# Kernel optimization log

Measured on AMD Instinct MI355X. Metric: run time of the kernel, lower is better.

The kernel has to match this reference:

```python
import jax, jax.numpy as jnp
import numpy as np

HEADS = 16  # config.heads


def setup_inputs() -> dict:
    key = jax.random.key(0)
    k1, k2, k3, k4 = jax.random.split(key, 4)
    B, S, H = 2, 2048, 2048
    x = jax.random.normal(k1, (B, S, H), dtype=jnp.float32)
    w_qkv = jax.random.normal(k2, (H, 3 * H), dtype=jnp.float32) * 0.02
    b_qkv = jax.random.normal(k3, (3 * H,), dtype=jnp.float32) * 0.02
    w_o = jax.random.normal(k4, (H, H), dtype=jnp.float32) * 0.02
    return {"x": x, "w_qkv": w_qkv, "b_qkv": b_qkv, "w_o": w_o}


def reference(x, w_qkv, b_qkv, w_o):
    # pre_layer_norm=False path: plain linear QKV projection
    B, S, H = x.shape
    hd = H // HEADS  # head_size
    scale = 1.0 / jnp.sqrt(jnp.float32(hd))  # 1/norm_factor^2, use_mup=False
    qkv = x @ w_qkv + b_qkv  # [B, S, 3H]
    q, k, v = qkv[..., :H], qkv[..., H:2 * H], qkv[..., 2 * H:]

    def split_heads(t):  # [B,S,H] -> [B,heads,S,hd]
        return t.reshape(B, S, HEADS, hd).transpose(0, 2, 1, 3)

    qh, kh, vh = split_heads(q), split_heads(k), split_heads(v)
    # score_4d_matmul with triangular masking + scale
    scores = jnp.einsum('bhqd,bhkd->bhqk', qh, kh) * scale  # [B,h,S,S]
    causal = jnp.tril(jnp.ones((S, S), dtype=bool))
    scores = jnp.where(causal, scores, -jnp.inf)
    probs = jax.nn.softmax(scores, axis=-1)
    # context_4d_matmul -> merge heads back to [B,S,H]
    ctx = jnp.einsum('bhqk,bhkd->bhqd', probs, vh)
    ctx = ctx.transpose(0, 2, 1, 3).reshape(B, S, H)
    # vector_matmul with attn_ow (no bias in this path)
    out = ctx @ w_o
    return out
```

## Files before the change

### kernel.cpp

```cpp
#include <hip/hip_runtime.h>
#include <cstdint>
#include <cstddef>

typedef __attribute__((ext_vector_type(8))) short bf16x8;
typedef __attribute__((ext_vector_type(4))) float f32x4;
typedef __attribute__((ext_vector_type(4))) unsigned short ushort4_;

#define MFMA16(a, b, c) __builtin_amdgcn_mfma_f32_16x16x32_bf16((a), (b), (c), 0, 0, 0)

__device__ __forceinline__ unsigned short f2bf(float f) {
  union { float f; unsigned u; } c; c.f = f;
  unsigned r = c.u + 0x7fffu + ((c.u >> 16) & 1u);
  return (unsigned short)(r >> 16);
}

__device__ __forceinline__ void gl_lds16(const unsigned short* g, unsigned short* l) {
  __builtin_amdgcn_global_load_lds(
      (const __attribute__((address_space(1))) void*)g,
      (__attribute__((address_space(3))) void*)l, 16, 0, 0);
}

__global__ __launch_bounds__(256) void k_cvt(const float* __restrict__ x,
                                             unsigned short* __restrict__ y) {
  int i = blockIdx.x * 256 + threadIdx.x;
  float4 v = reinterpret_cast<const float4*>(x)[i];
  ushort4_ o;
  o.x = f2bf(v.x); o.y = f2bf(v.y); o.z = f2bf(v.z); o.w = f2bf(v.w);
  reinterpret_cast<ushort4_*>(y)[i] = o;
}

__global__ __launch_bounds__(256) void k_transpose_cvt(const float* __restrict__ W,
                                                       unsigned short* __restrict__ WT,
                                                       int N) {
  __shared__ unsigned short t[64][65];
  const int n0 = blockIdx.x * 64;
  const int k0 = blockIdx.y * 64;
  const int tid = threadIdx.x;
#pragma unroll
  for (int i = 0; i < 16; i++) {
    int li = tid + i * 256;
    int kk = li >> 6, nn = li & 63;
    t[kk][nn] = f2bf(W[(size_t)(k0 + kk) * N + (n0 + nn)]);
  }
  __syncthreads();
#pragma unroll
  for (int i = 0; i < 16; i++) {
    int li = tid + i * 256;
    int nn = li >> 6, kk = li & 63;
    WT[(size_t)(n0 + nn) * 2048 + (k0 + kk)] = t[kk][nn];
  }
}

template <int MODE>
__global__ __launch_bounds__(256) void k_gemm(const unsigned short* __restrict__ A,
                                              const unsigned short* __restrict__ Bt,
                                              const float* __restrict__ bias,
                                              unsigned short* __restrict__ qb,
                                              unsigned short* __restrict__ kb,
                                              unsigned short* __restrict__ vtb,
                                              float* __restrict__ outp) {
  __shared__ __align__(16) unsigned short As[128 * 64];
  __shared__ __align__(16) unsigned short Bs[128 * 64];
  const int tid = threadIdx.x;
  const int lane = tid & 63, wid = tid >> 6;
  const int quad = lane >> 4, l16 = lane & 15;
  const int wm = wid >> 1, wn = wid & 1;
  const int m0 = blockIdx.y * 128, n0 = blockIdx.x * 128;

  f32x4 acc[4][4];
#pragma unroll
  for (int i = 0; i < 4; i++)
#pragma unroll
    for (int j = 0; j < 4; j++) {
      f32x4 z = {0.f, 0.f, 0.f, 0.f};
      acc[i][j] = z;
    }

  for (int k0 = 0; k0 < 2048; k0 += 64) {
    __syncthreads();
#pragma unroll
    for (int i = 0; i < 4; i++) {
      int slotbase = wid * 64 + i * 256;
      int slot = slotbase + lane;
      int row = slot >> 3, chs = slot & 7, gch = chs ^ (row & 7);
      gl_lds16(A + (size_t)(m0 + row) * 2048 + k0 + gch * 8, &As[slotbase * 8]);
      gl_lds16(Bt + (size_t)(n0 + row) * 2048 + k0 + gch * 8, &Bs[slotbase * 8]);
    }
    __syncthreads();
#pragma unroll
    for (int kc = 0; kc < 2; kc++) {
      bf16x8 af[4], bfr[4];
#pragma unroll
      for (int mt = 0; mt < 4; mt++) {
        int r = wm * 64 + mt * 16 + l16;
        int ch = kc * 4 + quad;
        af[mt] = *reinterpret_cast<const bf16x8*>(&As[r * 64 + ((ch ^ (r & 7)) * 8)]);
      }
#pragma unroll
      for (int nt = 0; nt < 4; nt++) {
        int r = wn * 64 + nt * 16 + l16;
        int ch = kc * 4 + quad;
        bfr[nt] = *reinterpret_cast<const bf16x8*>(&Bs[r * 64 + ((ch ^ (r & 7)) * 8)]);
      }
#pragma unroll
      for (int mt = 0; mt < 4; mt++)
#pragma unroll
        for (int nt = 0; nt < 4; nt++)
          acc[mt][nt] = MFMA16(af[mt], bfr[nt], acc[mt][nt]);
    }
  }

  const int mbase = m0 + wm * 64;
  const int nbase = n0 + wn * 64;
  if (MODE == 0) {
#pragma unroll
    for (int nt = 0; nt < 4; nt++) {
      int n = nbase + nt * 16 + l16;
      float bv = bias[n];
      int seg = n >> 11;
      int h = (n >> 7) & 15;
      int d = n & 127;
#pragma unroll
      for (int mt = 0; mt < 4; mt++) {
        int mrow = mbase + mt * 16 + quad * 4;
        int b = mrow >> 11, s = mrow & 2047;
        if (seg == 2) {
          ushort4_ pk;
          pk.x = f2bf(acc[mt][nt][0] + bv);
          pk.y = f2bf(acc[mt][nt][1] + bv);
          pk.z = f2bf(acc[mt][nt][2] + bv);
          pk.w = f2bf(acc[mt][nt][3] + bv);
          *reinterpret_cast<ushort4_*>(vtb + ((size_t)(b * 16 + h) * 128 + d) * 2048 + s) = pk;
        } else {
          unsigned short* dst = (seg == 0 ? qb : kb);
          size_t base = (size_t)(b * 16 + h) * 2048;
#pragma unroll
          for (int rg = 0; rg < 4; rg++)
            dst[(base + (s + rg)) * 128 + d] = f2bf(acc[mt][nt][rg] + bv);
        }
      }
    }
  } else {
#pragma unroll
    for (int nt = 0; nt < 4; nt++) {
      int n = nbase + nt * 16 + l16;
#pragma unroll
      for (int mt = 0; mt < 4; mt++) {
        int mrow = mbase + mt * 16 + quad * 4;
#pragma unroll
        for (int rg = 0; rg < 4; rg++)
          outp[(size_t)(mrow + rg) * 2048 + n] = acc[mt][nt][rg];
      }
    }
  }
}

__global__ __launch_bounds__(512) void k_attn(const unsigned short* __restrict__ qb,
                                              const unsigned short* __restrict__ kb,
                                              const unsigned short* __restrict__ vtb,
                                              unsigned short* __restrict__ ctx) {
  __shared__ __align__(16) unsigned short Ks[2][64 * 128];
  __shared__ __align__(16) unsigned short Vs[2][128 * 64];
  __shared__ __align__(16) unsigned short Ps[128 * 64];
  const int qt = (gridDim.x - 1) - blockIdx.x;
  const int bh = blockIdx.y;
  const int tid = threadIdx.x;
  const int lane = tid & 63, w = tid >> 6;
  const int quad = lane >> 4, l16 = lane & 15;
  const int qbase = qt * 128;
  const unsigned short* Qh = qb + (size_t)bh * 2048 * 128;
  const unsigned short* Kh = kb + (size_t)bh * 2048 * 128;
  const unsigned short* Vh = vtb + (size_t)bh * 128 * 2048;

  const int q_lo = qbase + w * 16;
  const int nkv = 2 * qt + 2;
  const float sl2 = 0.12751741f;

  bf16x8 qf[4];
#pragma unroll
  for (int kc = 0; kc < 4; kc++)
    qf[kc] = *reinterpret_cast<const bf16x8*>(
        Qh + (size_t)(q_lo + l16) * 128 + kc * 32 + quad * 8);

  f32x4 o[8];
#pragma unroll
  for (int dt = 0; dt < 8; dt++) {
    f32x4 z = {0.f, 0.f, 0.f, 0.f};
    o[dt] = z;
  }
  float m_run = -1e30f, l_run = 0.f;

  auto stage = [&](int kvb, int bsel) {
    unsigned short* Kd = &Ks[bsel][0];
    unsigned short* Vd = &Vs[bsel][0];
#pragma unroll
    for (int i = 0; i < 2; i++) {
      int slotbase = i * 512 + w * 64;
      int slot = slotbase + lane;
      int rowk = slot >> 4, chk = (slot & 15) ^ (rowk & 7);
      gl_lds16(Kh + (size_t)(kvb + rowk) * 128 + chk * 8, Kd + slotbase * 8);
      int rowv = slot >> 3, chv = (slot & 7) ^ (rowv & 7);
      gl_lds16(Vh + (size_t)rowv * 2048 + kvb + chv * 8, Vd + slotbase * 8);
    }
  };

  stage(0, 0);

  for (int kv = 0; kv < nkv; kv++) {
    const int kvb = kv * 64;
    const int cur = kv & 1;
    asm volatile("s_waitcnt vmcnt(0)" ::: "memory");
    asm volatile("s_barrier" ::: "memory");
    if (kv + 1 < nkv) stage(kvb + 64, cur ^ 1);
    if (kvb > q_lo + 15) continue;

    const unsigned short* Kc = &Ks[cur][0];
    const unsigned short* Vc = &Vs[cur][0];

    f32x4 sacc[4];
#pragma unroll
    for (int nt = 0; nt < 4; nt++) {
      f32x4 z = {0.f, 0.f, 0.f, 0.f};
      sacc[nt] = z;
    }
#pragma unroll
    for (int kc = 0; kc < 4; kc++) {
      bf16x8 kf[4];
#pragma unroll
      for (int nt = 0; nt < 4; nt++) {
        int r = nt * 16 + l16, ch = kc * 4 + quad;
        kf[nt] = *reinterpret_cast<const bf16x8*>(&Kc[r * 128 + ((ch ^ (r & 7)) * 8)]);
      }
#pragma unroll
      for (int nt = 0; nt < 4; nt++)
        sacc[nt] = MFMA16(kf[nt], qf[kc], sacc[nt]);
    }

    const bool needmask = (kvb + 63) > q_lo;
    const int qabs = q_lo + l16;
    float tmax = -1e30f;
#pragma unroll
    for (int nt = 0; nt < 4; nt++)
#pragma unroll
      for (int rg = 0; rg < 4; rg++) {
        float v = sacc[nt][rg] * sl2;
        if (needmask && (kvb + nt * 16 + quad * 4 + rg) > qabs) v = -1e30f;
        sacc[nt][rg] = v;
        tmax = fmaxf(tmax, v);
      }
    tmax = fmaxf(tmax, __shfl_xor(tmax, 16));
    tmax = fmaxf(tmax, __shfl_xor(tmax, 32));
    float mnew = fmaxf(m_run, tmax);
    float alpha = exp2f(m_run - mnew);
    m_run = mnew;
    float rsum = 0.f;
#pragma unroll
    for (int nt = 0; nt < 4; nt++)
#pragma unroll
      for (int rg = 0; rg < 4; rg++) {
        float p = exp2f(sacc[nt][rg] - mnew);
        sacc[nt][rg] = p;
        rsum += p;
      }
    rsum += __shfl_xor(rsum, 16);
    rsum += __shfl_xor(rsum, 32);
    l_run = l_run * alpha + rsum;
#pragma unroll
    for (int dt = 0; dt < 8; dt++)
#pragma unroll
      for (int rg = 0; rg < 4; rg++) o[dt][rg] *= alpha;

#pragma unroll
    for (int nt = 0; nt < 4; nt++) {
      ushort4_ pk;
      pk.x = f2bf(sacc[nt][0]);
      pk.y = f2bf(sacc[nt][1]);
      pk.z = f2bf(sacc[nt][2]);
      pk.w = f2bf(sacc[nt][3]);
      int chunk = nt * 2 + (quad >> 1);
      *reinterpret_cast<ushort4_*>(
          &Ps[(w * 16 + l16) * 64 + ((chunk ^ (l16 & 7)) * 8) + (quad & 1) * 4]) = pk;
    }
    asm volatile("s_waitcnt lgkmcnt(0)" ::: "memory");

#pragma unroll
    for (int kc = 0; kc < 2; kc++) {
      int chunkr = kc * 4 + quad;
      bf16x8 pf = *reinterpret_cast<const bf16x8*>(
          &Ps[(w * 16 + l16) * 64 + ((chunkr ^ (l16 & 7)) * 8)]);
#pragma unroll
      for (int dt = 0; dt < 8; dt++) {
        int r = dt * 16 + l16, ch = kc * 4 + quad;
        bf16x8 vf = *reinterpret_cast<const bf16x8*>(&Vc[r * 64 + ((ch ^ (r & 7)) * 8)]);
        o[dt] = MFMA16(vf, pf, o[dt]);
      }
    }
  }

  const int b = bh >> 4, h = bh & 15;
  const float inv = 1.f / l_run;
  const int s = q_lo + l16;
#pragma unroll
  for (int dt = 0; dt < 8; dt++) {
    int d0 = dt * 16 + quad * 4;
    ushort4_ pk;
    pk.x = f2bf(o[dt][0] * inv);
    pk.y = f2bf(o[dt][1] * inv);
    pk.z = f2bf(o[dt][2] * inv);
    pk.w = f2bf(o[dt][3] * inv);
    *reinterpret_cast<ushort4_*>(
        &ctx[((size_t)b * 2048 + s) * 2048 + h * 128 + d0]) = pk;
  }
}

extern "C" void kernel_launch(void* const* d_in, const int* in_sizes, int n_in,
                              void* d_out, int out_size, void* d_ws, size_t ws_size,
                              hipStream_t stream) {
  const float* x = (const float*)d_in[0];
  const float* w_qkv = (const float*)d_in[1];
  const float* b_qkv = (const float*)d_in[2];
  const float* w_o = (const float*)d_in[3];
  float* outp = (float*)d_out;

  unsigned short* ws = (unsigned short*)d_ws;
  unsigned short* xb    = ws;
  unsigned short* wqkvT = xb + 8388608;
  unsigned short* woT   = wqkvT + 12582912;
  unsigned short* qbuf  = woT + 4194304;
  unsigned short* kbuf  = qbuf + 8388608;
  unsigned short* vtbuf = kbuf + 8388608;
  unsigned short* ctxb  = vtbuf + 8388608;

  k_cvt<<<8192, 256, 0, stream>>>(x, xb);
  k_transpose_cvt<<<dim3(96, 32), 256, 0, stream>>>(w_qkv, wqkvT, 6144);
  k_transpose_cvt<<<dim3(32, 32), 256, 0, stream>>>(w_o, woT, 2048);
  k_gemm<0><<<dim3(48, 32), 256, 0, stream>>>(xb, wqkvT, b_qkv, qbuf, kbuf, vtbuf, nullptr);
  k_attn<<<dim3(16, 32), 512, 0, stream>>>(qbuf, kbuf, vtbuf, ctxb);
  k_gemm<1><<<dim3(16, 32), 256, 0, stream>>>(ctxb, woT, nullptr, nullptr, nullptr, nullptr, outp);
}
```

Measured before the change: 425.1 us.

## Give each attention wave two query tiles; merge prep kernels into one launch

The attention kernel now runs 4 waves of 256 threads instead of 8. Each wave handles 32 query rows as two 16-row halves, so every K and V fragment read from LDS feeds two MFMAs, halving LDS traffic per FLOP. Staging loops are widened to match. The three conversion and transpose kernels are fused into a single k_prep launch to cut launch overhead. The cost is higher register pressure per wave and fewer waves per block to hide latency, with launch_bounds(256,2) asking for two blocks per CU.

```diff
diff --git a/kernel.cpp b/kernel.cpp
--- a/kernel.cpp
+++ b/kernel.cpp
@@ -20,22 +20,35 @@
       (__attribute__((address_space(3))) void*)l, 16, 0, 0);
 }
 
-__global__ __launch_bounds__(256) void k_cvt(const float* __restrict__ x,
-                                             unsigned short* __restrict__ y) {
-  int i = blockIdx.x * 256 + threadIdx.x;
-  float4 v = reinterpret_cast<const float4*>(x)[i];
-  ushort4_ o;
-  o.x = f2bf(v.x); o.y = f2bf(v.y); o.z = f2bf(v.z); o.w = f2bf(v.w);
-  reinterpret_cast<ushort4_*>(y)[i] = o;
-}
-
-__global__ __launch_bounds__(256) void k_transpose_cvt(const float* __restrict__ W,
-                                                       unsigned short* __restrict__ WT,
-                                                       int N) {
+__global__ __launch_bounds__(256) void k_prep(const float* __restrict__ x,
+                                              unsigned short* __restrict__ xb,
+                                              const float* __restrict__ wqkv,
+                                              unsigned short* __restrict__ wqkvT,
+                                              const float* __restrict__ wo,
+                                              unsigned short* __restrict__ woT) {
   __shared__ unsigned short t[64][65];
-  const int n0 = blockIdx.x * 64;
-  const int k0 = blockIdx.y * 64;
+  const int blk = blockIdx.x;
   const int tid = threadIdx.x;
+  if (blk < 8192) {
+    int i = blk * 256 + tid;
+    float4 v = reinterpret_cast<const float4*>(x)[i];
+    ushort4_ o;
+    o.x = f2bf(v.x); o.y = f2bf(v.y); o.z = f2bf(v.z); o.w = f2bf(v.w);
+    reinterpret_cast<ushort4_*>(xb)[i] = o;
+    return;
+  }
+  const float* W;
+  unsigned short* WT;
+  int n0, k0, N;
+  if (blk < 11264) {
+    int local = blk - 8192;
+    W = wqkv; WT = wqkvT; N = 6144;
+    n0 = (local % 96) * 64; k0 = (local / 96) * 64;
+  } else {
+    int local = blk - 11264;
+    W = wo; WT = woT; N = 2048;
+    n0 = (local % 32) * 64; k0 = (local / 32) * 64;
+  }
 #pragma unroll
   for (int i = 0; i < 16; i++) {
     int li = tid + i * 256;
@@ -155,10 +168,10 @@
   }
 }
 
-__global__ __launch_bounds__(512) void k_attn(const unsigned short* __restrict__ qb,
-                                              const unsigned short* __restrict__ kb,
-                                              const unsigned short* __restrict__ vtb,
-                                              unsigned short* __restrict__ ctx) {
+__global__ __launch_bounds__(256, 2) void k_attn(const unsigned short* __restrict__ qb,
+                                                 const unsigned short* __restrict__ kb,
+                                                 const unsigned short* __restrict__ vtb,
+                                                 unsigned short* __restrict__ ctx) {
   __shared__ __align__(16) unsigned short Ks[2][64 * 128];
   __shared__ __align__(16) unsigned short Vs[2][128 * 64];
   __shared__ __align__(16) unsigned short Ps[128 * 64];
@@ -172,30 +185,34 @@
   const unsigned short* Kh = kb + (size_t)bh * 2048 * 128;
   const unsigned short* Vh = vtb + (size_t)bh * 128 * 2048;
 
-  const int q_lo = qbase + w * 16;
+  const int q_lo = qbase + w * 32;
   const int nkv = 2 * qt + 2;
   const float sl2 = 0.12751741f;
 
-  bf16x8 qf[4];
-#pragma unroll
-  for (int kc = 0; kc < 4; kc++)
-    qf[kc] = *reinterpret_cast<const bf16x8*>(
-        Qh + (size_t)(q_lo + l16) * 128 + kc * 32 + quad * 8);
-
-  f32x4 o[8];
-#pragma unroll
-  for (int dt = 0; dt < 8; dt++) {
-    f32x4 z = {0.f, 0.f, 0.f, 0.f};
-    o[dt] = z;
-  }
-  float m_run = -1e30f, l_run = 0.f;
+  bf16x8 qf[2][4];
+#pragma unroll
+  for (int half = 0; half < 2; half++)
+#pragma unroll
+    for (int kc = 0; kc < 4; kc++)
+      qf[half][kc] = *reinterpret_cast<const bf16x8*>(
+          Qh + (size_t)(q_lo + half * 16 + l16) * 128 + kc * 32 + quad * 8);
+
+  f32x4 o[2][8];
+#pragma unroll
+  for (int half = 0; half < 2; half++)
+#pragma unroll
+    for (int dt = 0; dt < 8; dt++) {
+      f32x4 z = {0.f, 0.f, 0.f, 0.f};
+      o[half][dt] = z;
+    }
+  float m_run[2] = {-1e30f, -1e30f}, l_run[2] = {0.f, 0.f};
 
   auto stage = [&](int kvb, int bsel) {
     unsigned short* Kd = &Ks[bsel][0];
     unsigned short* Vd = &Vs[bsel][0];
 #pragma unroll
-    for (int i = 0; i < 2; i++) {
-      int slotbase = i * 512 + w * 64;
+    for (int i = 0; i < 4; i++) {
+      int slotbase = i * 256 + w * 64;
       int slot = slotbase + lane;
       int rowk = slot >> 4, chk = (slot & 15) ^ (rowk & 7);
       gl_lds16(Kh + (size_t)(kvb + rowk) * 128 + chk * 8, Kd + slotbase * 8);
@@ -212,104 +229,114 @@
     asm volatile("s_waitcnt vmcnt(0)" ::: "memory");
     asm volatile("s_barrier" ::: "memory");
     if (kv + 1 < nkv) stage(kvb + 64, cur ^ 1);
-    if (kvb > q_lo + 15) continue;
+    if (kvb > q_lo + 31) continue;
 
     const unsigned short* Kc = &Ks[cur][0];
     const unsigned short* Vc = &Vs[cur][0];
 
-    f32x4 sacc[4];
-#pragma unroll
-    for (int nt = 0; nt < 4; nt++) {
-      f32x4 z = {0.f, 0.f, 0.f, 0.f};
-      sacc[nt] = z;
-    }
+    f32x4 sacc[2][4];
+#pragma unroll
+    for (int half = 0; half < 2; half++)
+#pragma unroll
+      for (int nt = 0; nt < 4; nt++) {
+        f32x4 z = {0.f, 0.f, 0.f, 0.f};
+        sacc[half][nt] = z;
+      }
 #pragma unroll
     for (int kc = 0; kc < 4; kc++) {
-      bf16x8 kf[4];
 #pragma unroll
       for (int nt = 0; nt < 4; nt++) {
         int r = nt * 16 + l16, ch = kc * 4 + quad;
-        kf[nt] = *reinterpret_cast<const bf16x8*>(&Kc[r * 128 + ((ch ^ (r & 7)) * 8)]);
-      }
+        bf16x8 kf = *reinterpret_cast<const bf16x8*>(&Kc[r * 128 + ((ch ^ (r & 7)) * 8)]);
+        sacc[0][nt] = MFMA16(kf, qf[0][kc], sacc[0][nt]);
+        sacc[1][nt] = MFMA16(kf, qf[1][kc], sacc[1][nt]);
+      }
+    }
+
+    const bool needmask = (kvb + 63) > q_lo;
+#pragma unroll
+    for (int half = 0; half < 2; half++) {
+      const int qabs = q_lo + half * 16 + l16;
+      float tmax = -1e30f;
 #pragma unroll
       for (int nt = 0; nt < 4; nt++)
-        sacc[nt] = MFMA16(kf[nt], qf[kc], sacc[nt]);
-    }
-
-    const bool needmask = (kvb + 63) > q_lo;
-    const int qabs = q_lo + l16;
-    float tmax = -1e30f;
-#pragma unroll
-    for (int nt = 0; nt < 4; nt++)
-#pragma unroll
-      for (int rg = 0; rg < 4; rg++) {
-        float v = sacc[nt][rg] * sl2;
-        if (needmask && (kvb + nt * 16 + quad * 4 + rg) > qabs) v = -1e30f;
-        sacc[nt][rg] = v;
-        tmax = fmaxf(tmax, v);
-      }
-    tmax = fmaxf(tmax, __shfl_xor(tmax, 16));
-    tmax = fmaxf(tmax, __shfl_xor(tmax, 32));
-    float mnew = fmaxf(m_run, tmax);
-    float alpha = exp2f(m_run - mnew);
-    m_run = mnew;
-    float rsum = 0.f;
-#pragma unroll
-    for (int nt = 0; nt < 4; nt++)
-#pragma unroll
-      for (int rg = 0; rg < 4; rg++) {
-        float p = exp2f(sacc[nt][rg] - mnew);
-        sacc[nt][rg] = p;
-        rsum += p;
-      }
-    rsum += __shfl_xor(rsum, 16);
-    rsum += __shfl_xor(rsum, 32);
-    l_run = l_run * alpha + rsum;
-#pragma unroll
-    for (int dt = 0; dt < 8; dt++)
-#pragma unroll
-      for (int rg = 0; rg < 4; rg++) o[dt][rg] *= alpha;
-
-#pragma unroll
-    for (int nt = 0; nt < 4; nt++) {
-      ushort4_ pk;
-      pk.x = f2bf(sacc[nt][0]);
-      pk.y = f2bf(sacc[nt][1]);
-      pk.z = f2bf(sacc[nt][2]);
-      pk.w = f2bf(sacc[nt][3]);
-      int chunk = nt * 2 + (quad >> 1);
-      *reinterpret_cast<ushort4_*>(
-          &Ps[(w * 16 + l16) * 64 + ((chunk ^ (l16 & 7)) * 8) + (quad & 1) * 4]) = pk;
+#pragma unroll
+        for (int rg = 0; rg < 4; rg++) {
+          float v = sacc[half][nt][rg] * sl2;
+          if (needmask && (kvb + nt * 16 + quad * 4 + rg) > qabs) v = -1e30f;
+          sacc[half][nt][rg] = v;
+          tmax = fmaxf(tmax, v);
+        }
+      tmax = fmaxf(tmax, __shfl_xor(tmax, 16));
+      tmax = fmaxf(tmax, __shfl_xor(tmax, 32));
+      float mnew = fmaxf(m_run[half], tmax);
+      float alpha = exp2f(m_run[half] - mnew);
+      m_run[half] = mnew;
+      float rsum = 0.f;
+#pragma unroll
+      for (int nt = 0; nt < 4; nt++)
+#pragma unroll
+        for (int rg = 0; rg < 4; rg++) {
+          float p = exp2f(sacc[half][nt][rg] - mnew);
+          sacc[half][nt][rg] = p;
+          rsum += p;
+        }
+      rsum += __shfl_xor(rsum, 16);
+      rsum += __shfl_xor(rsum, 32);
+      l_run[half] = l_run[half] * alpha + rsum;
+#pragma unroll
+      for (int dt = 0; dt < 8; dt++)
+#pragma unroll
+        for (int rg = 0; rg < 4; rg++) o[half][dt][rg] *= alpha;
+
+#pragma unroll
+      for (int nt = 0; nt < 4; nt++) {
+        ushort4_ pk;
+        pk.x = f2bf(sacc[half][nt][0]);
+        pk.y = f2bf(sacc[half][nt][1]);
+        pk.z = f2bf(sacc[half][nt][2]);
+        pk.w = f2bf(sacc[half][nt][3]);
+        int chunk = nt * 2 + (quad >> 1);
+        *reinterpret_cast<ushort4_*>(
+            &Ps[(w * 32 + half * 16 + l16) * 64 + ((chunk ^ (l16 & 7)) * 8) +
+                (quad & 1) * 4]) = pk;
+      }
     }
     asm volatile("s_waitcnt lgkmcnt(0)" ::: "memory");
 
 #pragma unroll
     for (int kc = 0; kc < 2; kc++) {
       int chunkr = kc * 4 + quad;
-      bf16x8 pf = *reinterpret_cast<const bf16x8*>(
-          &Ps[(w * 16 + l16) * 64 + ((chunkr ^ (l16 & 7)) * 8)]);
+      bf16x8 pf0 = *reinterpret_cast<const bf16x8*>(
+          &Ps[(w * 32 + l16) * 64 + ((chunkr ^ (l16 & 7)) * 8)]);
+      bf16x8 pf1 = *reinterpret_cast<const bf16x8*>(
+          &Ps[(w * 32 + 16 + l16) * 64 + ((chunkr ^ (l16 & 7)) * 8)]);
 #pragma unroll
       for (int dt = 0; dt < 8; dt++) {
         int r = dt * 16 + l16, ch = kc * 4 + quad;
         bf16x8 vf = *reinterpret_cast<const bf16x8*>(&Vc[r * 64 + ((ch ^ (r & 7)) * 8)]);
-        o[dt] = MFMA16(vf, pf, o[dt]);
+        o[0][dt] = MFMA16(vf, pf0, o[0][dt]);
+        o[1][dt] = MFMA16(vf, pf1, o[1][dt]);
       }
     }
   }
 
   const int b = bh >> 4, h = bh & 15;
-  const float inv = 1.f / l_run;
-  const int s = q_lo + l16;
-#pragma unroll
-  for (int dt = 0; dt < 8; dt++) {
-    int d0 = dt * 16 + quad * 4;
-    ushort4_ pk;
-    pk.x = f2bf(o[dt][0] * inv);
-    pk.y = f2bf(o[dt][1] * inv);
-    pk.z = f2bf(o[dt][2] * inv);
-    pk.w = f2bf(o[dt][3] * inv);
-    *reinterpret_cast<ushort4_*>(
-        &ctx[((size_t)b * 2048 + s) * 2048 + h * 128 + d0]) = pk;
+#pragma unroll
+  for (int half = 0; half < 2; half++) {
+    const float inv = 1.f / l_run[half];
+    const int s = q_lo + half * 16 + l16;
+#pragma unroll
+    for (int dt = 0; dt < 8; dt++) {
+      int d0 = dt * 16 + quad * 4;
+      ushort4_ pk;
+      pk.x = f2bf(o[half][dt][0] * inv);
+      pk.y = f2bf(o[half][dt][1] * inv);
+      pk.z = f2bf(o[half][dt][2] * inv);
+      pk.w = f2bf(o[half][dt][3] * inv);
+      *reinterpret_cast<ushort4_*>(
+          &ctx[((size_t)b * 2048 + s) * 2048 + h * 128 + d0]) = pk;
+    }
   }
 }
 
@@ -331,10 +358,8 @@
   unsigned short* vtbuf = kbuf + 8388608;
   unsigned short* ctxb  = vtbuf + 8388608;
 
-  k_cvt<<<8192, 256, 0, stream>>>(x, xb);
-  k_transpose_cvt<<<dim3(96, 32), 256, 0, stream>>>(w_qkv, wqkvT, 6144);
-  k_transpose_cvt<<<dim3(32, 32), 256, 0, stream>>>(w_o, woT, 2048);
+  k_prep<<<12288, 256, 0, stream>>>(x, xb, w_qkv, wqkvT, w_o, woT);
   k_gemm<0><<<dim3(48, 32), 256, 0, stream>>>(xb, wqkvT, b_qkv, qbuf, kbuf, vtbuf, nullptr);
-  k_attn<<<dim3(16, 32), 512, 0, stream>>>(qbuf, kbuf, vtbuf, ctxb);
+  k_attn<<<dim3(16, 32), 256, 0, stream>>>(qbuf, kbuf, vtbuf, ctxb);
   k_gemm<1><<<dim3(16, 32), 256, 0, stream>>>(ctxb, woT, nullptr, nullptr, nullptr, nullptr, outp);
 }
```

After: 422.5 us. Within noise of the previous version (-0.6%).
